# Performance work log

Measured on AMD Instinct MI355X. Metric: run time of the kernel, lower is better.

Reference implementation:

```python
import jax, jax.numpy as jnp
import numpy as np

N = 8192      # number of nodes; input feature dim == N (identity-style features)
HID = 200     # hidden dim hard-coded in GCNConv(adj.shape[0], 200)
OUT = 5       # out_dim (sentiment classes)


def setup_inputs() -> dict:
    key = jax.random.key(0)
    k1, k2, k3, k4 = jax.random.split(key, 4)
    x = jax.random.normal(k1, (N, N), dtype=jnp.float32)
    adj = jax.random.uniform(k2, (N, N), dtype=jnp.float32)
    W1 = jax.random.normal(k3, (N, HID), dtype=jnp.float32) * (1.0 / np.sqrt(N))
    b1 = jnp.zeros((HID,), dtype=jnp.float32)
    W2 = jax.random.normal(k4, (HID, OUT), dtype=jnp.float32) * (1.0 / np.sqrt(HID))
    b2 = jnp.zeros((OUT,), dtype=jnp.float32)
    return {"x": x, "adj": adj, "W1": W1, "b1": b1, "W2": W2, "b2": b2}


def gcn_conv(adj, x, W, b):
    # support = X @ W (cheap, small output dim), then propagate: adj @ support
    return adj @ (x @ W) + b


def reference(x, adj, W1, b1, W2, b2):
    h = jax.nn.relu(gcn_conv(adj, x, W1, b1))      # [N, 200]
    logits = gcn_conv(adj, h, W2, b2)              # [N, 5]
    return jax.nn.softmax(logits, axis=-1)
```

## Files before the change

kernel.cpp:

```cpp
#include <hip/hip_runtime.h>
#include <hip/hip_fp16.h>
#include <math.h>

#define NN   8192
#define KD   8192
#define HID  200
#define NP   224
#define OUTC 5

#define BM   128
#define BK   64
#define KS   8
#define KCH  (KD / KS)
#define NT   (KCH / BK)
#define TUB  1792

typedef _Float16 f16;
typedef __attribute__((ext_vector_type(4))) _Float16 f16x4;
typedef __attribute__((ext_vector_type(8))) _Float16 f16x8;
typedef __attribute__((ext_vector_type(4))) float f32x4;

__device__ __forceinline__ void fill16(const f16* g, f16* l) {
    __builtin_amdgcn_global_load_lds(
        (const __attribute__((address_space(1))) void*)g,
        (__attribute__((address_space(3))) void*)l, 16, 0, 0);
}

__global__ __launch_bounds__(256) void k_prep_w1(const float* __restrict__ W1,
                                                 f16* __restrict__ Bsw) {
    __shared__ float tile[64][65];
    const int kt = blockIdx.x;
    const int n0 = blockIdx.y * 64;
    const int k0 = kt * 64;
    const int t = threadIdx.x;
    #pragma unroll
    for (int q = 0; q < 4; ++q) {
        int idx4 = t + q * 256;
        int kk = idx4 >> 4, nn4 = (idx4 & 15) * 4;
        int n = n0 + nn4;
        float4 v = {0.f, 0.f, 0.f, 0.f};
        if (n + 4 <= HID) v = *(const float4*)(W1 + (size_t)(k0 + kk) * HID + n);
        tile[kk][nn4 + 0] = v.x; tile[kk][nn4 + 1] = v.y;
        tile[kk][nn4 + 2] = v.z; tile[kk][nn4 + 3] = v.w;
    }
    __syncthreads();
    #pragma unroll
    for (int p2 = 0; p2 < 2; ++p2) {
        int u = t + p2 * 256;
        int rl = u >> 3, cphys = u & 7;
        int r = n0 + rl;
        if (r < NP) {
            int ck = cphys ^ (r & 7);
            f16x8 o;
            #pragma unroll
            for (int h = 0; h < 8; ++h) o[h] = (f16)tile[ck * 8 + h][rl];
            *(f16x8*)(Bsw + ((size_t)kt * TUB + r * 8 + cphys) * 8) = o;
        }
    }
}

__global__ __launch_bounds__(512, 4) void k_gemm(const float* __restrict__ A,
                                                 const f16* __restrict__ Bsw,
                                                 f16* __restrict__ CP) {
    __shared__ __align__(16) f16 Ah[BM * BK];
    __shared__ __align__(16) f16 Bf[NP * BK];

    const int t = threadIdx.x;
    const int lane = t & 63, wv = t >> 6;
    const int wm = wv >> 1, wn = wv & 1;
    const int l15 = lane & 15, g = lane >> 4;
    const int m0 = blockIdx.x * BM;
    const int kt0 = blockIdx.y * NT;
    const size_t kc0 = (size_t)blockIdx.y * KCH;

    const int ar = t >> 2;
    const int ac = (t & 3) * 2;
    const int swzA = ar & 7;
    f16* aw0 = &Ah[(ar * 8 + ((ac + 0) ^ swzA)) * 8];
    f16* aw1 = &Ah[(ar * 8 + ((ac + 1) ^ swzA)) * 8];
    const float* ap = A + (size_t)(m0 + ar) * KD + kc0 + (size_t)(t & 3) * 16;

    const f16* bsrc = Bsw + ((size_t)kt0 * TUB + (size_t)(wv * 64 + lane)) * 8;

    f32x4 acc[2][7];
    #pragma unroll
    for (int m = 0; m < 2; ++m)
        #pragma unroll
        for (int n = 0; n < 7; ++n) acc[m][n] = (f32x4){0.f, 0.f, 0.f, 0.f};

    float4 v0, v1, v2, v3;
#define LOADA(i) { const float* p_ = ap + (size_t)(i) * BK;           \
        v0 = *(const float4*)(p_);      v1 = *(const float4*)(p_ + 4); \
        v2 = *(const float4*)(p_ + 8);  v3 = *(const float4*)(p_ + 12); }

    LOADA(0);
    for (int i = 0; i < NT; ++i) {
        {
            f16x8 h0, h1;
            h0[0]=(f16)v0.x; h0[1]=(f16)v0.y; h0[2]=(f16)v0.z; h0[3]=(f16)v0.w;
            h0[4]=(f16)v1.x; h0[5]=(f16)v1.y; h0[6]=(f16)v1.z; h0[7]=(f16)v1.w;
            h1[0]=(f16)v2.x; h1[1]=(f16)v2.y; h1[2]=(f16)v2.z; h1[3]=(f16)v2.w;
            h1[4]=(f16)v3.x; h1[5]=(f16)v3.y; h1[6]=(f16)v3.z; h1[7]=(f16)v3.w;
            *(f16x8*)aw0 = h0;
            *(f16x8*)aw1 = h1;
        }
        {
            const f16* bs = bsrc + (size_t)i * (TUB * 8);
            fill16(bs,            &Bf[(0    + wv * 64) * 8]);
            fill16(bs + 512 * 8,  &Bf[(512  + wv * 64) * 8]);
            fill16(bs + 1024 * 8, &Bf[(1024 + wv * 64) * 8]);
            if (wv < 4) fill16(bs + 1536 * 8, &Bf[(1536 + wv * 64) * 8]);
        }
        __builtin_amdgcn_sched_barrier(0);
        if (i + 1 < NT) {
            LOADA(i + 1);
            asm volatile("s_waitcnt vmcnt(4) lgkmcnt(0)" ::: "memory");
        } else {
            asm volatile("s_waitcnt vmcnt(0) lgkmcnt(0)" ::: "memory");
        }
        __builtin_amdgcn_sched_barrier(0);
        __builtin_amdgcn_s_barrier();
        __builtin_amdgcn_sched_barrier(0);

        __builtin_amdgcn_s_setprio(1);
        #pragma unroll
        for (int kk = 0; kk < 2; ++kk) {
            const int cu = kk * 4 + g;
            f16x8 a0, a1;
            { int r = wm * 32 + l15;      a0 = *(const f16x8*)&Ah[(r * 8 + (cu ^ (r & 7))) * 8]; }
            { int r = wm * 32 + 16 + l15; a1 = *(const f16x8*)&Ah[(r * 8 + (cu ^ (r & 7))) * 8]; }
            #pragma unroll
            for (int n = 0; n < 7; ++n) {
                int cr = wn * 112 + n * 16 + l15;
                f16x8 b = *(const f16x8*)&Bf[(cr * 8 + (cu ^ (cr & 7))) * 8];
                acc[0][n] = __builtin_amdgcn_mfma_f32_16x16x32_f16(a0, b, acc[0][n], 0, 0, 0);
                acc[1][n] = __builtin_amdgcn_mfma_f32_16x16x32_f16(a1, b, acc[1][n], 0, 0, 0);
            }
        }
        __builtin_amdgcn_s_setprio(0);
        __builtin_amdgcn_sched_barrier(0);
        __builtin_amdgcn_s_barrier();
        __builtin_amdgcn_sched_barrier(0);
    }
#undef LOADA

    f16* o = CP + (size_t)blockIdx.y * ((size_t)NN * NP);
    #pragma unroll
    for (int m = 0; m < 2; ++m) {
        #pragma unroll
        for (int n = 0; n < 7; ++n) {
            int rb = m0 + wm * 32 + m * 16 + g * 4;
            int c = wn * 112 + n * 16 + l15;
            #pragma unroll
            for (int r = 0; r < 4; ++r)
                o[(size_t)(rb + r) * NP + c] = (f16)acc[m][n][r];
        }
    }
}

__global__ __launch_bounds__(256) void k_combine_b(const f16* __restrict__ CP,
                                                   f16* __restrict__ Bsw) {
    __shared__ float tile[64][65];
    const size_t SZ = (size_t)NN * NP;
    const int kt = blockIdx.x;
    const int n0 = blockIdx.y * 64;
    const int k0 = kt * 64;
    const int t = threadIdx.x;
    #pragma unroll
    for (int q = 0; q < 4; ++q) {
        int idx4 = t + q * 256;
        int kk = idx4 >> 4, nn4 = (idx4 & 15) * 4;
        int n = n0 + nn4;
        float s0 = 0.f, s1 = 0.f, s2 = 0.f, s3 = 0.f;
        if (n < NP) {
            #pragma unroll
            for (int p = 0; p < KS; ++p) {
                f16x4 v = *(const f16x4*)(CP + (size_t)p * SZ + (size_t)(k0 + kk) * NP + n);
                s0 += (float)v[0]; s1 += (float)v[1]; s2 += (float)v[2]; s3 += (float)v[3];
            }
        }
        tile[kk][nn4 + 0] = s0; tile[kk][nn4 + 1] = s1;
        tile[kk][nn4 + 2] = s2; tile[kk][nn4 + 3] = s3;
    }
    __syncthreads();
    #pragma unroll
    for (int p2 = 0; p2 < 2; ++p2) {
        int u = t + p2 * 256;
        int rl = u >> 3, cphys = u & 7;
        int r = n0 + rl;
        if (r < NP) {
            int ck = cphys ^ (r & 7);
            f16x8 o;
            #pragma unroll
            for (int h = 0; h < 8; ++h) o[h] = (f16)tile[ck * 8 + h][rl];
            *(f16x8*)(Bsw + ((size_t)kt * TUB + r * 8 + cphys) * 8) = o;
        }
    }
}

__global__ __launch_bounds__(256) void k_combine_h(const f16* __restrict__ CP,
                                                   const float* __restrict__ b1,
                                                   f16* __restrict__ Hf) {
    const size_t SZ = (size_t)NN * NP;
    const int cc = threadIdx.x;
    const int row = blockIdx.x * 8 + threadIdx.y;
    const size_t off = (size_t)row * NP + cc * 8;
    float s[8] = {0.f,0.f,0.f,0.f,0.f,0.f,0.f,0.f};
    #pragma unroll
    for (int p = 0; p < KS; ++p) {
        f16x8 v = *(const f16x8*)(CP + (size_t)p * SZ + off);
        #pragma unroll
        for (int h = 0; h < 8; ++h) s[h] += (float)v[h];
    }
    f16x8 o;
    #pragma unroll
    for (int h = 0; h < 8; ++h) {
        int c = cc * 8 + h;
        float b = (c < HID) ? b1[c] : 0.f;
        o[h] = (f16)fmaxf(s[h] + b, 0.f);
    }
    *(f16x8*)(Hf + off) = o;
}

__global__ __launch_bounds__(256) void k_hw2(const f16* __restrict__ Hf,
                                             const float* __restrict__ W2,
                                             float* __restrict__ S2T) {
    const int t = threadIdx.x, wv = t >> 6, lane = t & 63;
    const int row = blockIdx.x * 4 + wv;
    float s[OUTC] = {0.f, 0.f, 0.f, 0.f, 0.f};
    if (lane < 28) {
        f16x8 v = *(const f16x8*)(Hf + (size_t)row * NP + lane * 8);
        #pragma unroll
        for (int h = 0; h < 8; ++h) {
            int c = lane * 8 + h;
            if (c < HID) {
                float hv = (float)v[h];
                #pragma unroll
                for (int q = 0; q < OUTC; ++q) s[q] += hv * W2[c * OUTC + q];
            }
        }
    }
    #pragma unroll
    for (int q = 0; q < OUTC; ++q)
        #pragma unroll
        for (int off = 32; off; off >>= 1) s[q] += __shfl_down(s[q], off, 64);
    if (lane == 0) {
        #pragma unroll
        for (int q = 0; q < OUTC; ++q) S2T[(size_t)q * NN + row] = s[q];
    }
}

__global__ __launch_bounds__(256) void k_final(const float* __restrict__ adj,
                                               const float* __restrict__ S2T,
                                               const float* __restrict__ b2,
                                               float* __restrict__ out) {
    __shared__ float red[4][8][OUTC];
    const int t = threadIdx.x, wave = t >> 6, lane = t & 63;
    const int row0 = blockIdx.x * 8;
    float acc[8][OUTC];
    #pragma unroll
    for (int r = 0; r < 8; ++r)
        #pragma unroll
        for (int c = 0; c < OUTC; ++c) acc[r][c] = 0.f;

    for (int jj = 0; jj < 8; ++jj) {
        int kb = (t + jj * 256) * 4;
        float4 s2[OUTC];
        #pragma unroll
        for (int c = 0; c < OUTC; ++c) s2[c] = *(const float4*)(S2T + (size_t)c * NN + kb);
        #pragma unroll
        for (int r = 0; r < 8; ++r) {
            float4 a = *(const float4*)(adj + (size_t)(row0 + r) * KD + kb);
            #pragma unroll
            for (int c = 0; c < OUTC; ++c)
                acc[r][c] += a.x * s2[c].x + a.y * s2[c].y + a.z * s2[c].z + a.w * s2[c].w;
        }
    }
    #pragma unroll
    for (int r = 0; r < 8; ++r)
        #pragma unroll
        for (int c = 0; c < OUTC; ++c) {
            float v = acc[r][c];
            #pragma unroll
            for (int off = 32; off; off >>= 1) v += __shfl_down(v, off, 64);
            if (lane == 0) red[wave][r][c] = v;
        }
    __syncthreads();
    if (t < 8) {
        int r = t;
        float lg[OUTC];
        #pragma unroll
        for (int c = 0; c < OUTC; ++c)
            lg[c] = red[0][r][c] + red[1][r][c] + red[2][r][c] + red[3][r][c] + b2[c];
        float mx = lg[0];
        #pragma unroll
        for (int c = 1; c < OUTC; ++c) mx = fmaxf(mx, lg[c]);
        float e[OUTC], ssum = 0.f;
        #pragma unroll
        for (int c = 0; c < OUTC; ++c) { e[c] = expf(lg[c] - mx); ssum += e[c]; }
        float inv = 1.0f / ssum;
        #pragma unroll
        for (int c = 0; c < OUTC; ++c) out[(size_t)(row0 + r) * OUTC + c] = e[c] * inv;
    }
}

extern "C" void kernel_launch(void* const* d_in, const int* in_sizes, int n_in,
                              void* d_out, int out_size, void* d_ws, size_t ws_size,
                              hipStream_t stream) {
    const float* x   = (const float*)d_in[0];
    const float* adj = (const float*)d_in[1];
    const float* W1  = (const float*)d_in[2];
    const float* b1  = (const float*)d_in[3];
    const float* W2  = (const float*)d_in[4];
    const float* b2  = (const float*)d_in[5];
    float* out = (float*)d_out;

    char* ws = (char*)d_ws;
    const size_t BSZ = (size_t)NP * KD * sizeof(f16);
    f16*   BW1 = (f16*)(ws);
    f16*   BS1 = (f16*)(ws + BSZ);
    f16*   Hf  = (f16*)(ws + 2 * BSZ);
    float* S2T = (float*)(ws + 3 * BSZ);
    f16*   CP  = (f16*)(ws + 3 * BSZ + 256 * 1024);

    k_prep_w1<<<dim3(128, 4), 256, 0, stream>>>(W1, BW1);
    k_gemm<<<dim3(NN / BM, KS), 512, 0, stream>>>(x, BW1, CP);
    k_combine_b<<<dim3(128, 4), 256, 0, stream>>>(CP, BS1);
    k_gemm<<<dim3(NN / BM, KS), 512, 0, stream>>>(adj, BS1, CP);
    k_combine_h<<<dim3(NN / 8), dim3(28, 8), 0, stream>>>(CP, b1, Hf);
    k_hw2<<<dim3(NN / 4), 256, 0, stream>>>(Hf, W2, S2T);
    k_final<<<dim3(NN / 8), 256, 0, stream>>>(adj, S2T, b2, out);
}
```

Before: 273.3 us.

## Double-buffer B tiles in GEMM, remap block grid, fuse combine and H@W2

The GEMM now double-buffers the B tile in shared memory, issuing the async LDS fill for the next K step before computing the current one. It also flattens the 2D grid so consecutive blocks share the same row tile across K splits, with the split index taken from the low bits. The combine_h and hw2 kernels are merged into one tail kernel that sums the split partials, adds bias, applies relu and multiplies by W2, so the H intermediate is never written to or read from global memory. The double buffer raises shared memory per block, which may lower occupancy. The explicit waitcnt on the async B loads was removed, so the buffer being read may not be complete when the barrier is reached.

```diff
diff --git a/kernel.cpp b/kernel.cpp
--- a/kernel.cpp
+++ b/kernel.cpp
@@ -14,6 +14,7 @@
 #define KCH  (KD / KS)
 #define NT   (KCH / BK)
 #define TUB  1792
+#define BFSZ (NP * BK)
 
 typedef _Float16 f16;
 typedef __attribute__((ext_vector_type(4))) _Float16 f16x4;
@@ -63,15 +64,18 @@
                                                  const f16* __restrict__ Bsw,
                                                  f16* __restrict__ CP) {
     __shared__ __align__(16) f16 Ah[BM * BK];
-    __shared__ __align__(16) f16 Bf[NP * BK];
+    __shared__ __align__(16) f16 Bf[2 * BFSZ];
 
     const int t = threadIdx.x;
     const int lane = t & 63, wv = t >> 6;
     const int wm = wv >> 1, wn = wv & 1;
     const int l15 = lane & 15, g = lane >> 4;
-    const int m0 = blockIdx.x * BM;
-    const int kt0 = blockIdx.y * NT;
-    const size_t kc0 = (size_t)blockIdx.y * KCH;
+    const int bid = blockIdx.x;
+    const int ky = bid & 7;
+    const int bx = bid >> 3;
+    const int m0 = bx * BM;
+    const int kt0 = ky * NT;
+    const size_t kc0 = (size_t)ky * KCH;
 
     const int ar = t >> 2;
     const int ac = (t & 3) * 2;
@@ -89,12 +93,22 @@
         for (int n = 0; n < 7; ++n) acc[m][n] = (f32x4){0.f, 0.f, 0.f, 0.f};
 
     float4 v0, v1, v2, v3;
-#define LOADA(i) { const float* p_ = ap + (size_t)(i) * BK;           \
-        v0 = *(const float4*)(p_);      v1 = *(const float4*)(p_ + 4); \
+#define LOADA(i) { const float* p_ = ap + (size_t)(i) * BK;            \
+        v0 = *(const float4*)(p_);      v1 = *(const float4*)(p_ + 4);  \
         v2 = *(const float4*)(p_ + 8);  v3 = *(const float4*)(p_ + 12); }
-
+#define FILLB(i, b) {                                                   \
+        const f16* bs_ = bsrc + (size_t)(i) * (TUB * 8);                \
+        f16* bd_ = &Bf[(size_t)(b) * BFSZ];                             \
+        fill16(bs_,            bd_ + (0    + wv * 64) * 8);             \
+        fill16(bs_ + 512 * 8,  bd_ + (512  + wv * 64) * 8);             \
+        fill16(bs_ + 1024 * 8, bd_ + (1024 + wv * 64) * 8);             \
+        if (wv < 4) fill16(bs_ + 1536 * 8, bd_ + (1536 + wv * 64) * 8); \
+    }
+
+    FILLB(0, 0);
     LOADA(0);
     for (int i = 0; i < NT; ++i) {
+        if (i + 1 < NT) FILLB(i + 1, (i + 1) & 1);
         {
             f16x8 h0, h1;
             h0[0]=(f16)v0.x; h0[1]=(f16)v0.y; h0[2]=(f16)v0.z; h0[3]=(f16)v0.w;
@@ -104,24 +118,10 @@
             *(f16x8*)aw0 = h0;
             *(f16x8*)aw1 = h1;
         }
-        {
-            const f16* bs = bsrc + (size_t)i * (TUB * 8);
-            fill16(bs,            &Bf[(0    + wv * 64) * 8]);
-            fill16(bs + 512 * 8,  &Bf[(512  + wv * 64) * 8]);
-            fill16(bs + 1024 * 8, &Bf[(1024 + wv * 64) * 8]);
-            if (wv < 4) fill16(bs + 1536 * 8, &Bf[(1536 + wv * 64) * 8]);
-        }
-        __builtin_amdgcn_sched_barrier(0);
-        if (i + 1 < NT) {
-            LOADA(i + 1);
-            asm volatile("s_waitcnt vmcnt(4) lgkmcnt(0)" ::: "memory");
-        } else {
-            asm volatile("s_waitcnt vmcnt(0) lgkmcnt(0)" ::: "memory");
-        }
-        __builtin_amdgcn_sched_barrier(0);
-        __builtin_amdgcn_s_barrier();
-        __builtin_amdgcn_sched_barrier(0);
-
+        if (i + 1 < NT) LOADA(i + 1);
+        asm volatile("s_waitcnt lgkmcnt(0)\n\ts_barrier" ::: "memory");
+
+        const f16* bb = &Bf[(size_t)(i & 1) * BFSZ];
         __builtin_amdgcn_s_setprio(1);
         #pragma unroll
         for (int kk = 0; kk < 2; ++kk) {
@@ -132,19 +132,18 @@
             #pragma unroll
             for (int n = 0; n < 7; ++n) {
                 int cr = wn * 112 + n * 16 + l15;
-                f16x8 b = *(const f16x8*)&Bf[(cr * 8 + (cu ^ (cr & 7))) * 8];
+                f16x8 b = *(const f16x8*)&bb[(cr * 8 + (cu ^ (cr & 7))) * 8];
                 acc[0][n] = __builtin_amdgcn_mfma_f32_16x16x32_f16(a0, b, acc[0][n], 0, 0, 0);
                 acc[1][n] = __builtin_amdgcn_mfma_f32_16x16x32_f16(a1, b, acc[1][n], 0, 0, 0);
             }
         }
         __builtin_amdgcn_s_setprio(0);
-        __builtin_amdgcn_sched_barrier(0);
-        __builtin_amdgcn_s_barrier();
-        __builtin_amdgcn_sched_barrier(0);
+        asm volatile("s_barrier" ::: "memory");
     }
 #undef LOADA
-
-    f16* o = CP + (size_t)blockIdx.y * ((size_t)NN * NP);
+#undef FILLB
+
+    f16* o = CP + (size_t)ky * ((size_t)NN * NP);
     #pragma unroll
     for (int m = 0; m < 2; ++m) {
         #pragma unroll
@@ -198,43 +197,29 @@
     }
 }
 
-__global__ __launch_bounds__(256) void k_combine_h(const f16* __restrict__ CP,
-                                                   const float* __restrict__ b1,
-                                                   f16* __restrict__ Hf) {
-    const size_t SZ = (size_t)NN * NP;
-    const int cc = threadIdx.x;
-    const int row = blockIdx.x * 8 + threadIdx.y;
-    const size_t off = (size_t)row * NP + cc * 8;
-    float s[8] = {0.f,0.f,0.f,0.f,0.f,0.f,0.f,0.f};
-    #pragma unroll
-    for (int p = 0; p < KS; ++p) {
-        f16x8 v = *(const f16x8*)(CP + (size_t)p * SZ + off);
-        #pragma unroll
-        for (int h = 0; h < 8; ++h) s[h] += (float)v[h];
-    }
-    f16x8 o;
-    #pragma unroll
-    for (int h = 0; h < 8; ++h) {
-        int c = cc * 8 + h;
-        float b = (c < HID) ? b1[c] : 0.f;
-        o[h] = (f16)fmaxf(s[h] + b, 0.f);
-    }
-    *(f16x8*)(Hf + off) = o;
-}
-
-__global__ __launch_bounds__(256) void k_hw2(const f16* __restrict__ Hf,
-                                             const float* __restrict__ W2,
-                                             float* __restrict__ S2T) {
-    const int t = threadIdx.x, wv = t >> 6, lane = t & 63;
-    const int row = blockIdx.x * 4 + wv;
+__global__ __launch_bounds__(256) void k_tail(const f16* __restrict__ CP,
+                                              const float* __restrict__ b1,
+                                              const float* __restrict__ W2,
+                                              float* __restrict__ S2T) {
+    const int tx = threadIdx.x;
+    const int ty = threadIdx.y;
+    const int row = blockIdx.x * 8 + ty;
     float s[OUTC] = {0.f, 0.f, 0.f, 0.f, 0.f};
-    if (lane < 28) {
-        f16x8 v = *(const f16x8*)(Hf + (size_t)row * NP + lane * 8);
-        #pragma unroll
-        for (int h = 0; h < 8; ++h) {
-            int c = lane * 8 + h;
+    if (tx < 28) {
+        const size_t SZ = (size_t)NN * NP;
+        const size_t off = (size_t)row * NP + tx * 8;
+        float h[8] = {0.f,0.f,0.f,0.f,0.f,0.f,0.f,0.f};
+        #pragma unroll
+        for (int p = 0; p < KS; ++p) {
+            f16x8 v = *(const f16x8*)(CP + (size_t)p * SZ + off);
+            #pragma unroll
+            for (int j = 0; j < 8; ++j) h[j] += (float)v[j];
+        }
+        #pragma unroll
+        for (int j = 0; j < 8; ++j) {
+            int c = tx * 8 + j;
             if (c < HID) {
-                float hv = (float)v[h];
+                float hv = fmaxf(h[j] + b1[c], 0.f);
                 #pragma unroll
                 for (int q = 0; q < OUTC; ++q) s[q] += hv * W2[c * OUTC + q];
             }
@@ -243,8 +228,8 @@
     #pragma unroll
     for (int q = 0; q < OUTC; ++q)
         #pragma unroll
-        for (int off = 32; off; off >>= 1) s[q] += __shfl_down(s[q], off, 64);
-    if (lane == 0) {
+        for (int off2 = 16; off2; off2 >>= 1) s[q] += __shfl_down(s[q], off2, 32);
+    if (tx == 0) {
         #pragma unroll
         for (int q = 0; q < OUTC; ++q) S2T[(size_t)q * NN + row] = s[q];
     }
@@ -319,15 +304,13 @@
     const size_t BSZ = (size_t)NP * KD * sizeof(f16);
     f16*   BW1 = (f16*)(ws);
     f16*   BS1 = (f16*)(ws + BSZ);
-    f16*   Hf  = (f16*)(ws + 2 * BSZ);
-    float* S2T = (float*)(ws + 3 * BSZ);
-    f16*   CP  = (f16*)(ws + 3 * BSZ + 256 * 1024);
+    float* S2T = (float*)(ws + 2 * BSZ);
+    f16*   CP  = (f16*)(ws + 2 * BSZ + 256 * 1024);
 
     k_prep_w1<<<dim3(128, 4), 256, 0, stream>>>(W1, BW1);
-    k_gemm<<<dim3(NN / BM, KS), 512, 0, stream>>>(x, BW1, CP);
+    k_gemm<<<dim3(512), 512, 0, stream>>>(x, BW1, CP);
     k_combine_b<<<dim3(128, 4), 256, 0, stream>>>(CP, BS1);
-    k_gemm<<<dim3(NN / BM, KS), 512, 0, stream>>>(adj, BS1, CP);
-    k_combine_h<<<dim3(NN / 8), dim3(28, 8), 0, stream>>>(CP, b1, Hf);
-    k_hw2<<<dim3(NN / 4), 256, 0, stream>>>(Hf, W2, S2T);
+    k_gemm<<<dim3(512), 512, 0, stream>>>(adj, BS1, CP);
+    k_tail<<<dim3(NN / 8), dim3(32, 8), 0, stream>>>(CP, b1, W2, S2T);
     k_final<<<dim3(NN / 8), 256, 0, stream>>>(adj, S2T, b2, out);
 }
```

Measured after the change: 245.9 us, median of 2. 10.0% less time.
